# Optimization experiments

Measured on AMD Instinct MI355X. Metric: run time of the kernel, lower is better.

Reference implementation:

```python
import jax, jax.numpy as jnp
import numpy as np

B = 512
C = 256
HEADS = 16
DH = 16
SIGMA = 1e-4  # GaussianNoise(0.0001)
LEAK = 0.2


def _axial_attn(x, Wq, Wkv, Wo, bo, axis):
    # x: [B, 8, 4, 5, C]; attend along `axis`, folding other dims into batch.
    xm = jnp.moveaxis(x, axis, -2)                      # [..., T, C]
    q = xm @ Wq                                          # [..., T, C]
    kv = xm @ Wkv                                        # [..., T, 2C]
    k, v = kv[..., :C], kv[..., C:]
    hshape = q.shape[:-1] + (HEADS, DH)
    q = q.reshape(hshape)
    k = k.reshape(hshape)
    v = v.reshape(hshape)
    dots = jnp.einsum('...thd,...shd->...hts', q, k) * (DH ** -0.5)
    attn = jax.nn.softmax(dots, axis=-1)
    o = jnp.einsum('...hts,...shd->...thd', attn, v).reshape(xm.shape)
    o = o @ Wo + bo
    return jnp.moveaxis(o, -2, axis)


def setup_inputs() -> dict:
    key = jax.random.key(0)
    ks = jax.random.split(key, 12)
    inp = {
        'x': jax.random.normal(ks[0], (B, 8, 4, 5), jnp.float32),
        'noise': jax.random.normal(ks[1], (B, 8, 4, 5, 1), jnp.float32),
        'rand': jax.random.uniform(ks[2], (B, 8, 4, 5, 1), jnp.float32),
        # encoder Linear(2, 256, bias=False), stored as [in, out]
        'W_enc': jax.random.normal(ks[3], (2, C), jnp.float32) * (2 ** -0.5),
        # axial positional embedding (sum of per-axis params == one full param)
        'pos_emb': jax.random.normal(ks[4], (8, 4, 5, C), jnp.float32) * 0.02,
        # 2 AxialAttention layers x 3 axes of SelfAttention params
        'Wq': jax.random.normal(ks[5], (2, 3, C, C), jnp.float32) * (C ** -0.5),
        'Wkv': jax.random.normal(ks[6], (2, 3, C, 2 * C), jnp.float32) * (C ** -0.5),
        'Wo': jax.random.normal(ks[7], (2, 3, C, C), jnp.float32) * (C ** -0.5),
        'bo': jnp.zeros((2, 3, C), jnp.float32),
        # decoder Linear(256, 1, bias=True)
        'Wd': jax.random.normal(ks[8], (C, 1), jnp.float32) * (C ** -0.5),
        'bd': jnp.zeros((1,), jnp.float32),
    }
    return inp


def reference(x, noise, rand, W_enc, pos_emb, Wq, Wkv, Wo, bo, Wd, bd):
    h = x[..., None] + SIGMA * noise                  # unsqueeze + GaussianNoise
    h = jnp.concatenate([h, rand], axis=-1)           # [B,8,4,5,2]
    h = jnp.tanh(h @ W_enc)                           # [B,8,4,5,256]
    h = h + pos_emb                                   # axial positional embedding
    for l in range(2):                                # two AxialAttention blocks
        h = (_axial_attn(h, Wq[l, 0], Wkv[l, 0], Wo[l, 0], bo[l, 0], 1)
             + _axial_attn(h, Wq[l, 1], Wkv[l, 1], Wo[l, 1], bo[l, 1], 2)
             + _axial_attn(h, Wq[l, 2], Wkv[l, 2], Wo[l, 2], bo[l, 2], 3))
        h = jnp.where(h >= 0, h, LEAK * h)            # LeakyReLU(0.2)
    out = jax.nn.sigmoid(h @ Wd + bd)                 # decoder Linear + Sigmoid
    return out[..., 0]                                # squeeze(-1) -> [B,8,4,5]
```

## Files before the change

### kernel.cpp

```cpp
#include <hip/hip_runtime.h>
#include <hip/hip_bf16.h>
#include <math.h>

#define NPOS 81920
#define CDIM 256
#define SIGMA 1e-4f
#define LEAK 0.2f

typedef __hip_bfloat16 bf16;
typedef __bf16 bf16x8 __attribute__((ext_vector_type(8)));
typedef float f32x4 __attribute__((ext_vector_type(4)));
typedef unsigned short u16x8 __attribute__((ext_vector_type(8)));

__device__ __forceinline__ float bf2f(unsigned short u) {
    return __uint_as_float(((unsigned)u) << 16);
}
__device__ __forceinline__ unsigned short f2bfu(float f) {
    bf16 h = __float2bfloat16(f);
    return *reinterpret_cast<unsigned short*>(&h);
}

__global__ void encode_kernel(const float* __restrict__ x, const float* __restrict__ noise,
                              const float* __restrict__ rnd, const float* __restrict__ We,
                              const float* __restrict__ pe, bf16* __restrict__ H) {
    int p = blockIdx.x;
    int c = threadIdx.x;
    float a = x[p] + SIGMA * noise[p];
    float b = rnd[p];
    float z = a * We[c] + b * We[CDIM + c];
    z = fminf(15.f, fmaxf(-15.f, z));
    float e = __expf(2.f * z);
    float th = 1.f - 2.f / (e + 1.f);
    H[(size_t)p * CDIM + c] = __float2bfloat16(th + pe[(p % 160) * CDIM + c]);
}

__global__ void bias3_kernel(const float* __restrict__ bo, float* __restrict__ bsum) {
    int l = blockIdx.x, c = threadIdx.x;
    bsum[l * CDIM + c] = bo[l * 768 + c] + bo[l * 768 + 256 + c] + bo[l * 768 + 512 + c];
}

__global__ void pack_qkv_kernel(const float* __restrict__ Wq, const float* __restrict__ Wkv,
                                bf16* __restrict__ out) {
    int mat = blockIdx.x / 768;
    int n = blockIdx.x % 768;
    int k = threadIdx.x;
    float v = (n < 256) ? Wq[(size_t)mat * 65536 + (size_t)k * 256 + n]
                        : Wkv[(size_t)mat * 131072 + (size_t)k * 512 + (n - 256)];
    out[(size_t)blockIdx.x * 256 + k] = __float2bfloat16(v);
}
__global__ void pack_wo_kernel(const float* __restrict__ Wo, bf16* __restrict__ out) {
    int l = blockIdx.x / 256;
    int n = blockIdx.x % 256;
    int ck = threadIdx.x;
    for (int a = 0; a < 3; a++)
        out[(size_t)(l * 256 + n) * 768 + a * 256 + ck] =
            __float2bfloat16(Wo[(((size_t)(l * 3 + a)) * 256 + ck) * 256 + n]);
}

__global__ __launch_bounds__(256, 2) void step_kernel(
    const bf16* __restrict__ Hg, const bf16* __restrict__ Wqkv, bf16* __restrict__ QKV,
    const bf16* __restrict__ O, const bf16* __restrict__ WoTl, bf16* __restrict__ Hnw,
    const float* __restrict__ bias, int nW, int nMblk) {
    __shared__ __bf16 smem[32768];
    int tid = threadIdx.x;
    int wave = tid >> 6, lane = tid & 63;
    int quad = lane >> 4, m = lane & 15;

    if (blockIdx.x >= nW) {
        __bf16* As = smem;
        __bf16* Bs = smem + 8192;
        int bid = blockIdx.x - nW;
        int xcd = bid & 7, slot = bid >> 3;
        int g = slot / 9;
        int nb = slot - g * 9;
        int mb = xcd + 8 * g;
        int bm = mb * 128, bn = nb * 256;
        int wr = (wave >> 1) * 64, wc = (wave & 1) * 128;
        f32x4 acc[4][8] = {};

#define STAGE_G(buf, k0)                                                                       \
    {                                                                                          \
        _Pragma("unroll") for (int rep = 0; rep < 2; rep++) {                                  \
            int ch = rep * 256 + wave * 64 + lane;                                             \
            int row = ch >> 2, cc = ch & 3, gc = cc ^ ((row >> 1) & 3);                        \
            __builtin_amdgcn_global_load_lds(                                                  \
                (const __attribute__((address_space(1))) void*)(Hg + (size_t)(bm + row) * CDIM \
                                                                + (k0) + gc * 8),              \
                (__attribute__((address_space(3))) void*)(As + (buf) * 4096                    \
                                                          + (rep * 256 + wave * 64) * 8),      \
                16, 0, 0);                                                                     \
        }                                                                                      \
        _Pragma("unroll") for (int rep = 0; rep < 4; rep++) {                                  \
            int ch = rep * 256 + wave * 64 + lane;                                             \
            int row = ch >> 2, cc = ch & 3, gc = cc ^ ((row >> 1) & 3);                        \
            __builtin_amdgcn_global_load_lds(                                                  \
                (const __attribute__((address_space(1))) void*)(Wqkv + (size_t)(bn + row) * 256\
                                                                + (k0) + gc * 8),              \
                (__attribute__((address_space(3))) void*)(Bs + (buf) * 8192                    \
                                                          + (rep * 256 + wave * 64) * 8),      \
                16, 0, 0);                                                                     \
        }                                                                                      \
    }

        STAGE_G(0, 0);
#pragma unroll
        for (int it = 0; it < 8; it++) {
            __syncthreads();
            if (it < 7) STAGE_G((it + 1) & 1, (it + 1) * 32);
            const __bf16* Ab = As + (it & 1) * 4096;
            const __bf16* Bb = Bs + (it & 1) * 8192;
            bf16x8 af[4], bfr[8];
#pragma unroll
            for (int i = 0; i < 4; i++) {
                int r = wr + i * 16 + m;
                af[i] = *(const bf16x8*)(Ab + r * 32 + ((quad ^ ((r >> 1) & 3)) * 8));
            }
#pragma unroll
            for (int j = 0; j < 8; j++) {
                int r = wc + j * 16 + m;
                bfr[j] = *(const bf16x8*)(Bb + r * 32 + ((quad ^ ((r >> 1) & 3)) * 8));
            }
#pragma unroll
            for (int i = 0; i < 4; i++)
#pragma unroll
                for (int j = 0; j < 8; j++)
                    acc[i][j] = __builtin_amdgcn_mfma_f32_16x16x32_bf16(af[i], bfr[j], acc[i][j], 0, 0, 0);
        }
#undef STAGE_G

        __syncthreads();
        {
            unsigned short* ct = (unsigned short*)smem;
#pragma unroll
            for (int i = 0; i < 4; i++)
#pragma unroll
                for (int j = 0; j < 8; j++)
#pragma unroll
                    for (int r = 0; r < 4; r++) {
                        int row = wr + i * 16 + quad * 4 + r;
                        int col = wc + j * 16 + m;
                        ct[row * 256 + (col ^ (((row >> 2) & 3) << 4))] = f2bfu(acc[i][j][r]);
                    }
            __syncthreads();
#pragma unroll
            for (int p = 0; p < 16; p++) {
                int chunk = p * 256 + tid;
                int row = chunk >> 5, c8 = (chunk & 31) * 8;
                ulonglong2 v = *(const ulonglong2*)(ct + row * 256
                                                    + (c8 ^ (((row >> 2) & 3) << 4)));
                *(ulonglong2*)((unsigned short*)QKV + (size_t)(bm + row) * 2304 + bn + c8) = v;
            }
        }
    } else {
        __bf16* As = smem;
        __bf16* Bs = smem + 16384;
        int bid = blockIdx.x;
        int xcd = bid & 7, slot = bid >> 3;
        int g = slot >> 1;
        int nb = slot & 1;
        int mb = xcd + 8 * g;
        int bm = mb * 128, bn = nb * 128;
        int wr = (wave >> 1) * 64, wc = (wave & 1) * 64;
        f32x4 acc[4][4] = {};

#define STAGE_W(buf, k0)                                                                       \
    {                                                                                          \
        _Pragma("unroll") for (int rep = 0; rep < 4; rep++) {                                  \
            int ch = rep * 256 + wave * 64 + lane;                                             \
            int row = ch >> 3, cc = ch & 7, gc = cc ^ (row & 7);                               \
            __builtin_amdgcn_global_load_lds(                                                  \
                (const __attribute__((address_space(1))) void*)(O + (size_t)(bm + row) * 768   \
                                                                + (k0) + gc * 8),              \
                (__attribute__((address_space(3))) void*)(As + (buf) * 8192                    \
                                                          + (rep * 256 + wave * 64) * 8),      \
                16, 0, 0);                                                                     \
        }                                                                                      \
        _Pragma("unroll") for (int rep = 0; rep < 4; rep++) {                                  \
            int ch = rep * 256 + wave * 64 + lane;                                             \
            int row = ch >> 3, cc = ch & 7, gc = cc ^ (row & 7);                               \
            __builtin_amdgcn_global_load_lds(                                                  \
                (const __attribute__((address_space(1))) void*)(WoTl + (size_t)(bn + row) * 768\
                                                                + (k0) + gc * 8),              \
                (__attribute__((address_space(3))) void*)(Bs + (buf) * 8192                    \
                                                          + (rep * 256 + wave * 64) * 8),      \
                16, 0, 0);                                                                     \
        }                                                                                      \
    }

        STAGE_W(0, 0);
#pragma unroll
        for (int it = 0; it < 12; it++) {
            __syncthreads();
            if (it < 11) STAGE_W((it + 1) & 1, (it + 1) * 64);
            const __bf16* Ab = As + (it & 1) * 8192;
            const __bf16* Bb = Bs + (it & 1) * 8192;
#pragma unroll
            for (int kk = 0; kk < 2; kk++) {
                bf16x8 af[4], bfr[4];
#pragma unroll
                for (int i = 0; i < 4; i++) {
                    int r = wr + i * 16 + m, cix = kk * 4 + quad;
                    af[i] = *(const bf16x8*)(Ab + r * 64 + ((cix ^ (r & 7)) * 8));
                }
#pragma unroll
                for (int j = 0; j < 4; j++) {
                    int r = wc + j * 16 + m, cix = kk * 4 + quad;
                    bfr[j] = *(const bf16x8*)(Bb + r * 64 + ((cix ^ (r & 7)) * 8));
                }
#pragma unroll
                for (int i = 0; i < 4; i++)
#pragma unroll
                    for (int j = 0; j < 4; j++)
                        acc[i][j] = __builtin_amdgcn_mfma_f32_16x16x32_bf16(af[i], bfr[j], acc[i][j], 0, 0, 0);
            }
        }
#undef STAGE_W

        __syncthreads();
        {
            unsigned short* ct = (unsigned short*)smem;
#pragma unroll
            for (int i = 0; i < 4; i++)
#pragma unroll
                for (int j = 0; j < 4; j++)
#pragma unroll
                    for (int r = 0; r < 4; r++) {
                        int row = wr + i * 16 + quad * 4 + r;
                        int lcol = wc + j * 16 + m;
                        float v = acc[i][j][r] + bias[bn + lcol];
                        v = v >= 0.f ? v : LEAK * v;
                        ct[row * 128 + (lcol ^ (((row >> 2) & 3) << 4))] = f2bfu(v);
                    }
            __syncthreads();
#pragma unroll
            for (int p = 0; p < 8; p++) {
                int chunk = p * 256 + tid;
                int row = chunk >> 4, c8 = (chunk & 15) * 8;
                ulonglong2 v = *(const ulonglong2*)(ct + row * 128
                                                    + (c8 ^ (((row >> 2) & 3) << 4)));
                *(ulonglong2*)((unsigned short*)Hnw + (size_t)(bm + row) * CDIM + bn + c8) = v;
            }
        }
    }
}

template <int AXIS>
__device__ __forceinline__ void attn_axis(const bf16* __restrict__ QKV, bf16* __restrict__ O,
                                          int seq, int hl) {
    constexpr int T      = (AXIS == 0) ? 8 : (AXIS == 1) ? 4 : 5;
    constexpr int STRIDE = (AXIS == 0) ? 20 : (AXIS == 1) ? 5 : 1;
    int base;
    if (AXIS == 0)      { int b = seq / 20, r = seq % 20; base = b * 160 + r; }
    else if (AXIS == 1) { int b = seq / 40, r = seq % 40; base = b * 160 + (r / 5) * 20 + (r % 5); }
    else                { int b = seq / 32, r = seq % 32; base = b * 160 + r * 5; }

    const unsigned short* qbase =
        (const unsigned short*)QKV + (size_t)base * 2304 + AXIS * 768 + hl * 8;
    float k[T][8], v[T][8];
#pragma unroll
    for (int t = 0; t < T; t++) {
        const unsigned short* rowp = qbase + (size_t)t * STRIDE * 2304;
        u16x8 ku = *(const u16x8*)(rowp + 256);
        u16x8 vu = *(const u16x8*)(rowp + 512);
#pragma unroll
        for (int i = 0; i < 8; i++) { k[t][i] = bf2f(ku[i]); v[t][i] = bf2f(vu[i]); }
    }

#pragma unroll
    for (int t = 0; t < T; t++) {
        u16x8 qu = *(const u16x8*)(qbase + (size_t)t * STRIDE * 2304);
        float q[8];
#pragma unroll
        for (int i = 0; i < 8; i++) q[i] = bf2f(qu[i]);
        float sc[T];
#pragma unroll
        for (int s = 0; s < T; s++) {
            float p = q[0] * k[s][0] + q[1] * k[s][1] + q[2] * k[s][2] + q[3] * k[s][3]
                    + q[4] * k[s][4] + q[5] * k[s][5] + q[6] * k[s][6] + q[7] * k[s][7];
            p += __shfl_xor(p, 1);
            sc[s] = p * 0.25f;
        }
        float mx = sc[0];
#pragma unroll
        for (int s = 1; s < T; s++) mx = fmaxf(mx, sc[s]);
        float sum = 0.f;
#pragma unroll
        for (int s = 0; s < T; s++) { sc[s] = __expf(sc[s] - mx); sum += sc[s]; }
        float inv = 1.f / sum;
        float o[8] = {};
#pragma unroll
        for (int s = 0; s < T; s++)
#pragma unroll
            for (int i = 0; i < 8; i++) o[i] += sc[s] * v[s][i];
        u16x8 st;
#pragma unroll
        for (int i = 0; i < 8; i++) st[i] = f2bfu(o[i] * inv);
        *(u16x8*)((unsigned short*)O + (size_t)(base + t * STRIDE) * 768 + AXIS * 256 + hl * 8) = st;
    }
}

__global__ __launch_bounds__(256) void attn_all(const bf16* __restrict__ QKV,
                                                bf16* __restrict__ O, int n0, int n1) {
    int wave = threadIdx.x >> 6, lane = threadIdx.x & 63;
    int sub = wave * 2 + (lane >> 5);
    int hl = lane & 31;
    int blk = blockIdx.x;
    if (blk < n0)            attn_axis<0>(QKV, O, blk * 8 + sub, hl);
    else if (blk < n0 + n1)  attn_axis<1>(QKV, O, (blk - n0) * 8 + sub, hl);
    else                     attn_axis<2>(QKV, O, (blk - n0 - n1) * 8 + sub, hl);
}

__global__ void decode_kernel(const bf16* __restrict__ H, const float* __restrict__ Wd,
                              const float* __restrict__ bd, float* __restrict__ out) {
    int tid = threadIdx.x;
    int pos = blockIdx.x * 4 + (tid >> 6);
    int lane = tid & 63;
    float acc = 0.f;
#pragma unroll
    for (int q = 0; q < 4; q++) {
        int c = lane + q * 64;
        acc += __bfloat162float(H[(size_t)pos * CDIM + c]) * Wd[c];
    }
#pragma unroll
    for (int off = 32; off > 0; off >>= 1) acc += __shfl_down(acc, off);
    if (lane == 0) out[pos] = 1.f / (1.f + __expf(-(acc + bd[0])));
}

extern "C" void kernel_launch(void* const* d_in, const int* in_sizes, int n_in,
                              void* d_out, int out_size, void* d_ws, size_t ws_size,
                              hipStream_t stream) {
    const float* x     = (const float*)d_in[0];
    const float* noise = (const float*)d_in[1];
    const float* rnd   = (const float*)d_in[2];
    const float* We    = (const float*)d_in[3];
    const float* pe    = (const float*)d_in[4];
    const float* Wq    = (const float*)d_in[5];
    const float* Wkv   = (const float*)d_in[6];
    const float* Wo    = (const float*)d_in[7];
    const float* bo    = (const float*)d_in[8];
    const float* Wd    = (const float*)d_in[9];
    const float* bd    = (const float*)d_in[10];
    float* out = (float*)d_out;

    bf16* H0    = (bf16*)d_ws;
    bf16* H1    = H0 + (size_t)NPOS * CDIM;
    bf16* WqkvT = H1 + (size_t)NPOS * CDIM;
    bf16* WoT   = WqkvT + (size_t)2 * 2304 * 256;
    float* bsum = (float*)(WoT + (size_t)2 * 256 * 768);
    bf16* QKV   = (bf16*)(bsum + 512);

    size_t fixed = ((size_t)2 * NPOS * CDIM + (size_t)2 * 2304 * 256 + (size_t)2 * 256 * 768) * 2
                   + 512 * 4;
    int c = 4;
    while (c < 64 && fixed + (size_t)(NPOS / c) * (2304 + 768) * 2 > ws_size) c <<= 1;
    int mc = NPOS / c;
    bf16* O = QKV + (size_t)mc * 2304;
    bf16* Hbuf[3] = { H0, H1, H0 };

    pack_qkv_kernel<<<6 * 768, 256, 0, stream>>>(Wq, Wkv, WqkvT);
    pack_wo_kernel<<<2 * 256, 256, 0, stream>>>(Wo, WoT);
    bias3_kernel<<<2, 256, 0, stream>>>(bo, bsum);
    encode_kernel<<<NPOS, 256, 0, stream>>>(x, noise, rnd, We, pe, H0);

    int nMblk = mc / 128;
    int cells = mc / 160;
    int n0 = cells * 20 / 8, n1 = cells * 40 / 8, n2 = cells * 32 / 8;
    int TT = 2 * c;

    for (int t = 0; t <= TT; t++) {
        int gG = (t < TT) ? nMblk * 9 : 0;
        int gW = (t >= 1) ? nMblk * 2 : 0;
        const bf16 *Hg = nullptr, *Wq_ = nullptr;
        if (gG) {
            int lg = t / c, cg = t % c;
            Hg = Hbuf[lg] + (size_t)cg * mc * CDIM;
            Wq_ = WqkvT + (size_t)lg * 2304 * 256;
        }
        const bf16* WoTl = nullptr; bf16* Hnw = nullptr; const float* bs = nullptr;
        if (gW) {
            int tw = t - 1, lw = tw / c, cw = tw % c;
            WoTl = WoT + (size_t)lw * 256 * 768;
            Hnw = Hbuf[lw + 1] + (size_t)cw * mc * CDIM;
            bs = bsum + lw * CDIM;
        }
        step_kernel<<<gG + gW, 256, 0, stream>>>(Hg, Wq_, QKV, O, WoTl, Hnw, bs, gW, nMblk);
        if (t < TT) attn_all<<<n0 + n1 + n2, 256, 0, stream>>>(QKV, O, n0, n1);
    }

    decode_kernel<<<NPOS / 4, 256, 0, stream>>>(Hbuf[2], Wd, bd, out);
}
```

Baseline: 640.5 us.

## Fuse attention into step kernel as a three-stage software pipeline with double-buffered QKV/O

```diff
diff --git a/kernel.cpp b/kernel.cpp
--- a/kernel.cpp
+++ b/kernel.cpp
@@ -57,19 +57,90 @@
             __float2bfloat16(Wo[(((size_t)(l * 3 + a)) * 256 + ck) * 256 + n]);
 }
 
+template <int AXIS>
+__device__ __forceinline__ void attn_axis(const bf16* __restrict__ QKV, bf16* __restrict__ O,
+                                          int seq, int hl) {
+    constexpr int T      = (AXIS == 0) ? 8 : (AXIS == 1) ? 4 : 5;
+    constexpr int STRIDE = (AXIS == 0) ? 20 : (AXIS == 1) ? 5 : 1;
+    int base;
+    if (AXIS == 0)      { int b = seq / 20, r = seq % 20; base = b * 160 + r; }
+    else if (AXIS == 1) { int b = seq / 40, r = seq % 40; base = b * 160 + (r / 5) * 20 + (r % 5); }
+    else                { int b = seq / 32, r = seq % 32; base = b * 160 + r * 5; }
+
+    const unsigned short* qbase =
+        (const unsigned short*)QKV + (size_t)base * 2304 + AXIS * 768 + hl * 8;
+    float k[T][8], v[T][8];
+#pragma unroll
+    for (int t = 0; t < T; t++) {
+        const unsigned short* rowp = qbase + (size_t)t * STRIDE * 2304;
+        u16x8 ku = *(const u16x8*)(rowp + 256);
+        u16x8 vu = *(const u16x8*)(rowp + 512);
+#pragma unroll
+        for (int i = 0; i < 8; i++) { k[t][i] = bf2f(ku[i]); v[t][i] = bf2f(vu[i]); }
+    }
+
+#pragma unroll
+    for (int t = 0; t < T; t++) {
+        u16x8 qu = *(const u16x8*)(qbase + (size_t)t * STRIDE * 2304);
+        float q[8];
+#pragma unroll
+        for (int i = 0; i < 8; i++) q[i] = bf2f(qu[i]);
+        float sc[T];
+#pragma unroll
+        for (int s = 0; s < T; s++) {
+            float p = q[0] * k[s][0] + q[1] * k[s][1] + q[2] * k[s][2] + q[3] * k[s][3]
+                    + q[4] * k[s][4] + q[5] * k[s][5] + q[6] * k[s][6] + q[7] * k[s][7];
+            p += __shfl_xor(p, 1);
+            sc[s] = p * 0.25f;
+        }
+        float mx = sc[0];
+#pragma unroll
+        for (int s = 1; s < T; s++) mx = fmaxf(mx, sc[s]);
+        float sum = 0.f;
+#pragma unroll
+        for (int s = 0; s < T; s++) { sc[s] = __expf(sc[s] - mx); sum += sc[s]; }
+        float inv = 1.f / sum;
+        float o[8] = {};
+#pragma unroll
+        for (int s = 0; s < T; s++)
+#pragma unroll
+            for (int i = 0; i < 8; i++) o[i] += sc[s] * v[s][i];
+        u16x8 st;
+#pragma unroll
+        for (int i = 0; i < 8; i++) st[i] = f2bfu(o[i] * inv);
+        *(u16x8*)((unsigned short*)O + (size_t)(base + t * STRIDE) * 768 + AXIS * 256 + hl * 8) = st;
+    }
+}
+
 __global__ __launch_bounds__(256, 2) void step_kernel(
     const bf16* __restrict__ Hg, const bf16* __restrict__ Wqkv, bf16* __restrict__ QKV,
     const bf16* __restrict__ O, const bf16* __restrict__ WoTl, bf16* __restrict__ Hnw,
-    const float* __restrict__ bias, int nW, int nMblk) {
+    const float* __restrict__ bias,
+    const bf16* __restrict__ QKVr, bf16* __restrict__ Oa,
+    int nWu, int nGu, int nAu, int n0, int n1) {
     __shared__ __bf16 smem[32768];
     int tid = threadIdx.x;
     int wave = tid >> 6, lane = tid & 63;
     int quad = lane >> 4, m = lane & 15;
-
-    if (blockIdx.x >= nW) {
+    int uid = blockIdx.x >> 3, l8 = blockIdx.x & 7;
+
+    if (uid >= nWu) {
+        int rem = uid - nWu;
+        int tot = nGu + nAu;
+        int au = rem * nAu / tot;
+        bool isA = ((rem + 1) * nAu / tot) > au;
+        if (isA) {
+            int blk = au * 8 + l8;
+            int sub = wave * 2 + (lane >> 5);
+            int hl = lane & 31;
+            if (blk < n0)            attn_axis<0>(QKVr, Oa, blk * 8 + sub, hl);
+            else if (blk < n0 + n1)  attn_axis<1>(QKVr, Oa, (blk - n0) * 8 + sub, hl);
+            else                     attn_axis<2>(QKVr, Oa, (blk - n0 - n1) * 8 + sub, hl);
+            return;
+        }
         __bf16* As = smem;
         __bf16* Bs = smem + 8192;
-        int bid = blockIdx.x - nW;
+        int bid = (rem - au) * 8 + l8;
         int xcd = bid & 7, slot = bid >> 3;
         int g = slot / 9;
         int nb = slot - g * 9;
@@ -139,15 +210,14 @@
                     for (int r = 0; r < 4; r++) {
                         int row = wr + i * 16 + quad * 4 + r;
                         int col = wc + j * 16 + m;
-                        ct[row * 256 + (col ^ (((row >> 2) & 3) << 4))] = f2bfu(acc[i][j][r]);
+                        ct[row * 256 + col] = f2bfu(acc[i][j][r]);
                     }
             __syncthreads();
 #pragma unroll
             for (int p = 0; p < 16; p++) {
                 int chunk = p * 256 + tid;
                 int row = chunk >> 5, c8 = (chunk & 31) * 8;
-                ulonglong2 v = *(const ulonglong2*)(ct + row * 256
-                                                    + (c8 ^ (((row >> 2) & 3) << 4)));
+                ulonglong2 v = *(const ulonglong2*)(ct + row * 256 + c8);
                 *(ulonglong2*)((unsigned short*)QKV + (size_t)(bm + row) * 2304 + bn + c8) = v;
             }
         }
@@ -229,85 +299,18 @@
                         int lcol = wc + j * 16 + m;
                         float v = acc[i][j][r] + bias[bn + lcol];
                         v = v >= 0.f ? v : LEAK * v;
-                        ct[row * 128 + (lcol ^ (((row >> 2) & 3) << 4))] = f2bfu(v);
+                        ct[row * 128 + lcol] = f2bfu(v);
                     }
             __syncthreads();
 #pragma unroll
             for (int p = 0; p < 8; p++) {
                 int chunk = p * 256 + tid;
                 int row = chunk >> 4, c8 = (chunk & 15) * 8;
-                ulonglong2 v = *(const ulonglong2*)(ct + row * 128
-                                                    + (c8 ^ (((row >> 2) & 3) << 4)));
+                ulonglong2 v = *(const ulonglong2*)(ct + row * 128 + c8);
                 *(ulonglong2*)((unsigned short*)Hnw + (size_t)(bm + row) * CDIM + bn + c8) = v;
             }
         }
     }
-}
-
-template <int AXIS>
-__device__ __forceinline__ void attn_axis(const bf16* __restrict__ QKV, bf16* __restrict__ O,
-                                          int seq, int hl) {
-    constexpr int T      = (AXIS == 0) ? 8 : (AXIS == 1) ? 4 : 5;
-    constexpr int STRIDE = (AXIS == 0) ? 20 : (AXIS == 1) ? 5 : 1;
-    int base;
-    if (AXIS == 0)      { int b = seq / 20, r = seq % 20; base = b * 160 + r; }
-    else if (AXIS == 1) { int b = seq / 40, r = seq % 40; base = b * 160 + (r / 5) * 20 + (r % 5); }
-    else                { int b = seq / 32, r = seq % 32; base = b * 160 + r * 5; }
-
-    const unsigned short* qbase =
-        (const unsigned short*)QKV + (size_t)base * 2304 + AXIS * 768 + hl * 8;
-    float k[T][8], v[T][8];
-#pragma unroll
-    for (int t = 0; t < T; t++) {
-        const unsigned short* rowp = qbase + (size_t)t * STRIDE * 2304;
-        u16x8 ku = *(const u16x8*)(rowp + 256);
-        u16x8 vu = *(const u16x8*)(rowp + 512);
-#pragma unroll
-        for (int i = 0; i < 8; i++) { k[t][i] = bf2f(ku[i]); v[t][i] = bf2f(vu[i]); }
-    }
-
-#pragma unroll
-    for (int t = 0; t < T; t++) {
-        u16x8 qu = *(const u16x8*)(qbase + (size_t)t * STRIDE * 2304);
-        float q[8];
-#pragma unroll
-        for (int i = 0; i < 8; i++) q[i] = bf2f(qu[i]);
-        float sc[T];
-#pragma unroll
-        for (int s = 0; s < T; s++) {
-            float p = q[0] * k[s][0] + q[1] * k[s][1] + q[2] * k[s][2] + q[3] * k[s][3]
-                    + q[4] * k[s][4] + q[5] * k[s][5] + q[6] * k[s][6] + q[7] * k[s][7];
-            p += __shfl_xor(p, 1);
-            sc[s] = p * 0.25f;
-        }
-        float mx = sc[0];
-#pragma unroll
-        for (int s = 1; s < T; s++) mx = fmaxf(mx, sc[s]);
-        float sum = 0.f;
-#pragma unroll
-        for (int s = 0; s < T; s++) { sc[s] = __expf(sc[s] - mx); sum += sc[s]; }
-        float inv = 1.f / sum;
-        float o[8] = {};
-#pragma unroll
-        for (int s = 0; s < T; s++)
-#pragma unroll
-            for (int i = 0; i < 8; i++) o[i] += sc[s] * v[s][i];
-        u16x8 st;
-#pragma unroll
-        for (int i = 0; i < 8; i++) st[i] = f2bfu(o[i] * inv);
-        *(u16x8*)((unsigned short*)O + (size_t)(base + t * STRIDE) * 768 + AXIS * 256 + hl * 8) = st;
-    }
-}
-
-__global__ __launch_bounds__(256) void attn_all(const bf16* __restrict__ QKV,
-                                                bf16* __restrict__ O, int n0, int n1) {
-    int wave = threadIdx.x >> 6, lane = threadIdx.x & 63;
-    int sub = wave * 2 + (lane >> 5);
-    int hl = lane & 31;
-    int blk = blockIdx.x;
-    if (blk < n0)            attn_axis<0>(QKV, O, blk * 8 + sub, hl);
-    else if (blk < n0 + n1)  attn_axis<1>(QKV, O, (blk - n0) * 8 + sub, hl);
-    else                     attn_axis<2>(QKV, O, (blk - n0 - n1) * 8 + sub, hl);
 }
 
 __global__ void decode_kernel(const bf16* __restrict__ H, const float* __restrict__ Wd,
@@ -347,14 +350,16 @@
     bf16* WqkvT = H1 + (size_t)NPOS * CDIM;
     bf16* WoT   = WqkvT + (size_t)2 * 2304 * 256;
     float* bsum = (float*)(WoT + (size_t)2 * 256 * 768);
-    bf16* QKV   = (bf16*)(bsum + 512);
+    bf16* QKV0  = (bf16*)(bsum + 512);
 
     size_t fixed = ((size_t)2 * NPOS * CDIM + (size_t)2 * 2304 * 256 + (size_t)2 * 256 * 768) * 2
                    + 512 * 4;
     int c = 4;
-    while (c < 64 && fixed + (size_t)(NPOS / c) * (2304 + 768) * 2 > ws_size) c <<= 1;
+    while (c < 64 && fixed + (size_t)(NPOS / c) * (2304 + 768) * 2 * 2 > ws_size) c <<= 1;
     int mc = NPOS / c;
-    bf16* O = QKV + (size_t)mc * 2304;
+    bf16* QKV1 = QKV0 + (size_t)mc * 2304;
+    bf16* O0   = QKV1 + (size_t)mc * 2304;
+    bf16* O1   = O0 + (size_t)mc * 768;
     bf16* Hbuf[3] = { H0, H1, H0 };
 
     pack_qkv_kernel<<<6 * 768, 256, 0, stream>>>(Wq, Wkv, WqkvT);
@@ -365,26 +370,38 @@
     int nMblk = mc / 128;
     int cells = mc / 160;
     int n0 = cells * 20 / 8, n1 = cells * 40 / 8, n2 = cells * 32 / 8;
+    int nA = n0 + n1 + n2;
     int TT = 2 * c;
 
-    for (int t = 0; t <= TT; t++) {
-        int gG = (t < TT) ? nMblk * 9 : 0;
-        int gW = (t >= 1) ? nMblk * 2 : 0;
-        const bf16 *Hg = nullptr, *Wq_ = nullptr;
-        if (gG) {
+    for (int t = 0; t <= TT + 1; t++) {
+        int nGu = (t < TT) ? (nMblk * 9) >> 3 : 0;
+        int nAu = (t >= 1 && t <= TT) ? nA >> 3 : 0;
+        int nWu = (t >= 2) ? (nMblk * 2) >> 3 : 0;
+
+        const bf16 *HgP = nullptr, *WqP = nullptr; bf16* QKVw = nullptr;
+        if (nGu) {
             int lg = t / c, cg = t % c;
-            Hg = Hbuf[lg] + (size_t)cg * mc * CDIM;
-            Wq_ = WqkvT + (size_t)lg * 2304 * 256;
-        }
-        const bf16* WoTl = nullptr; bf16* Hnw = nullptr; const float* bs = nullptr;
-        if (gW) {
-            int tw = t - 1, lw = tw / c, cw = tw % c;
+            HgP  = Hbuf[lg] + (size_t)cg * mc * CDIM;
+            WqP  = WqkvT + (size_t)lg * 2304 * 256;
+            QKVw = (t & 1) ? QKV1 : QKV0;
+        }
+        const bf16* QKVr = nullptr; bf16* Oaw = nullptr;
+        if (nAu) {
+            int ta = t - 1;
+            QKVr = (ta & 1) ? QKV1 : QKV0;
+            Oaw  = (ta & 1) ? O1 : O0;
+        }
+        const bf16* Ord = nullptr; const bf16* WoTl = nullptr;
+        bf16* Hnw = nullptr; const float* bs = nullptr;
+        if (nWu) {
+            int tw = t - 2, lw = tw / c, cw = tw % c;
+            Ord  = (tw & 1) ? O1 : O0;
             WoTl = WoT + (size_t)lw * 256 * 768;
-            Hnw = Hbuf[lw + 1] + (size_t)cw * mc * CDIM;
-            bs = bsum + lw * CDIM;
-        }
-        step_kernel<<<gG + gW, 256, 0, stream>>>(Hg, Wq_, QKV, O, WoTl, Hnw, bs, gW, nMblk);
-        if (t < TT) attn_all<<<n0 + n1 + n2, 256, 0, stream>>>(QKV, O, n0, n1);
+            Hnw  = Hbuf[lw + 1] + (size_t)cw * mc * CDIM;
+            bs   = bsum + lw * CDIM;
+        }
+        step_kernel<<<(nWu + nGu + nAu) * 8, 256, 0, stream>>>(
+            HgP, WqP, QKVw, Ord, WoTl, Hnw, bs, QKVr, Oaw, nWu, nGu, nAu, n0, n1);
     }
 
     decode_kernel<<<NPOS / 4, 256, 0, stream>>>(Hbuf[2], Wd, bd, out);
```

New measurement: 745.8 us. +16.5%, slower.
